# Kernel tuning notes

Hardware: AMD Instinct MI355X
Metric: run time of the kernel (lower is better)

The kernel has to match this reference:

```python
import jax, jax.numpy as jnp
import numpy as np
import math

S, B, F, D, H, L, DFF, PRED = 448, 64, 8, 256, 8, 4, 256, 96
DK = D // H
EPS = 1e-5


def _pos_enc(length, d_model):
    pos = jnp.arange(length, dtype=jnp.float32)[:, None]            # [S,1]
    div = jnp.exp(jnp.arange(0, d_model, 2, dtype=jnp.float32) * (-math.log(10000.0) / d_model))
    pe = jnp.zeros((length, d_model), jnp.float32)
    pe = pe.at[:, 0::2].set(jnp.sin(pos * div))
    pe = pe.at[:, 1::2].set(jnp.cos(pos * div))
    return pe[:, None, :]                                            # [S,1,D]


def _layernorm(x, g, b):
    mu = jnp.mean(x, axis=-1, keepdims=True)
    var = jnp.mean((x - mu) ** 2, axis=-1, keepdims=True)
    return (x - mu) / jnp.sqrt(var + EPS) * g + b


def setup_inputs() -> dict:
    key = jax.random.key(0)
    ks = jax.random.split(key, 12)
    g = lambda k, shape: (jax.random.normal(k, shape) * 0.02).astype(jnp.float32)
    return {
        "src": jax.random.normal(ks[0], (S, B, F), jnp.float32),
        "w_in": g(ks[1], (F, D)), "b_in": jnp.zeros((D,), jnp.float32),
        "Wq": g(ks[2], (L, D, D)), "bq": jnp.zeros((L, D), jnp.float32),
        "Wk": g(ks[3], (L, D, D)), "bk": jnp.zeros((L, D), jnp.float32),
        "Wv": g(ks[4], (L, D, D)), "bv": jnp.zeros((L, D), jnp.float32),
        "Wo": g(ks[5], (L, D, D)), "bo": jnp.zeros((L, D), jnp.float32),
        "g1": jnp.ones((L, D), jnp.float32), "be1": jnp.zeros((L, D), jnp.float32),
        "W1": g(ks[6], (L, D, DFF)), "b1": jnp.zeros((L, DFF), jnp.float32),
        "W2": g(ks[7], (L, DFF, D)), "b2": jnp.zeros((L, D), jnp.float32),
        "g2": jnp.ones((L, D), jnp.float32), "be2": jnp.zeros((L, D), jnp.float32),
        "w_out": g(ks[8], (D, F)), "b_out": jnp.zeros((F,), jnp.float32),
    }


def reference(src, w_in, b_in, Wq, bq, Wk, bk, Wv, bv, Wo, bo,
              g1, be1, W1, b1, W2, b2, g2, be2, w_out, b_out):
    x = src @ w_in + b_in                 # [S,B,D]
    x = x + _pos_enc(S, D)

    scale = math.sqrt(DK)

    def layer(x, p):
        wq, bq_, wk, bk_, wv, bv_, wo, bo_, g1_, be1_, w1, b1_, w2, b2_, g2_, be2_ = p
        Q = (x @ wq + bq_).reshape(S, B, H, DK)
        K = (x @ wk + bk_).reshape(S, B, H, DK)
        V = (x @ wv + bv_).reshape(S, B, H, DK)
        scores = jnp.einsum("sbhd,tbhd->bhst", Q, K) / scale   # [B,H,S,S]
        attn = jax.nn.softmax(scores, axis=-1)
        ctx = jnp.einsum("bhst,tbhd->sbhd", attn, V).reshape(S, B, D)
        x = _layernorm(x + (ctx @ wo + bo_), g1_, be1_)
        ff = jax.nn.relu(x @ w1 + b1_) @ w2 + b2_
        x = _layernorm(x + ff, g2_, be2_)
        return x, None

    x, _ = jax.lax.scan(layer, x, (Wq, bq, Wk, bk, Wv, bv, Wo, bo,
                                   g1, be1, W1, b1, W2, b2, g2, be2))
    return x[-PRED:] @ w_out + b_out      # [PRED,B,F]
```

## Files before the change

### kernel.cpp

```cpp
#include <hip/hip_runtime.h>
#include <hip/hip_bf16.h>
#include <math.h>

#define S_ 448
#define B_ 64
#define F_ 8
#define D_ 256
#define H_ 8
#define DK_ 32
#define L_ 4
#define PRED_ 96
#define NT_ (S_ * B_)
#define PANEL_ (S_ * DK_)
#define VTP_ (32 * 512)
#define SCQ_ 0.25503484f

typedef unsigned short bf16_t;
using bf16x8 = __attribute__((ext_vector_type(8))) short;
using f32x4  = __attribute__((ext_vector_type(4))) float;
using f32x16 = __attribute__((ext_vector_type(16))) float;

__device__ __forceinline__ float b2f(bf16_t b) {
  return __uint_as_float(((unsigned)b) << 16);
}
__device__ __forceinline__ bf16_t f2b(float f) {
  unsigned u = __float_as_uint(f);
  u += 0x7fffu + ((u >> 16) & 1u);
  return (bf16_t)(u >> 16);
}
__device__ __forceinline__ unsigned pk2(float lo, float hi) {
  union { __hip_bfloat162 h; unsigned u; } c;
  c.h = __float22bfloat162_rn(make_float2(lo, hi));
  return c.u;
}
__device__ __forceinline__ void gload16(const bf16_t* g, char* l) {
  __builtin_amdgcn_global_load_lds(
      (const __attribute__((address_space(1))) unsigned*)g,
      (__attribute__((address_space(3))) unsigned*)l, 16, 0, 0);
}

__global__ __launch_bounds__(256) void embed_kernel(
    const float* __restrict__ src, const float* __restrict__ w_in,
    const float* __restrict__ b_in, bf16_t* __restrict__ x) {
  int n = blockIdx.x;
  int d = threadIdx.x;
  const float* srow = src + (size_t)n * F_;
  float acc = b_in[d];
#pragma unroll
  for (int f = 0; f < F_; ++f) acc += srow[f] * w_in[f * D_ + d];
  int s = n / B_;
  int i2 = d & ~1;
  float freq = __expf(-9.210340371976184f * (float)i2 / (float)D_);
  float ang = (float)s * freq;
  float pe = (d & 1) ? cosf(ang) : sinf(ang);
  x[(size_t)n * D_ + d] = f2b(acc + pe);
}

__global__ __launch_bounds__(256) void transpose_w_kernel(
    const float* __restrict__ W, bf16_t* __restrict__ Wt, float scale) {
  __shared__ float t[32][33];
  int l = blockIdx.z;
  int k0 = blockIdx.x * 32, n0 = blockIdx.y * 32;
  int x = threadIdx.x, y = threadIdx.y;
  const float* src = W + ((size_t)l * 256 + k0) * 256 + n0;
#pragma unroll
  for (int i = y; i < 32; i += 8) t[i][x] = src[(size_t)i * 256 + x];
  __syncthreads();
  bf16_t* dst = Wt + ((size_t)l * 256 + n0) * 256 + k0;
#pragma unroll
  for (int i = y; i < 32; i += 8) dst[(size_t)i * 256 + x] = f2b(t[x][i] * scale);
}

__global__ __launch_bounds__(512) void vtrans_kernel(
    const bf16_t* __restrict__ V, bf16_t* __restrict__ Vt) {
  __shared__ bf16_t t[32][456];
  int bh = blockIdx.x, tid = threadIdx.x;
  const bf16_t* Vp = V + (size_t)bh * PANEL_;
#pragma unroll
  for (int p = 0; p < 4; ++p) {
    int idx = tid + p * 512;
    if (idx < 1792) {
      int s = idx >> 2, c = idx & 3;
      uint4 v = *(const uint4*)(Vp + s * 32 + c * 8);
      unsigned w[4] = {v.x, v.y, v.z, v.w};
#pragma unroll
      for (int e = 0; e < 8; ++e) {
        bf16_t val = (bf16_t)((e & 1) ? (w[e >> 1] >> 16) : (w[e >> 1] & 0xffff));
        *(bf16_t*)((char*)&t[0][0] + (c * 8 + e) * 912 + s * 2) = val;
      }
    }
  }
  __syncthreads();
  bf16_t* Op = Vt + (size_t)bh * VTP_;
#pragma unroll
  for (int p = 0; p < 4; ++p) {
    int idx = tid + p * 512;
    int dk = idx >> 6, sl = idx & 63;
    uint4 v = {0, 0, 0, 0};
    if (sl < 56) v = *(const uint4*)((char*)&t[0][0] + dk * 912 + sl * 16);
    *(uint4*)(Op + dk * 512 + sl * 8) = v;
  }
}

template <int ALAY, int OLAY, int RELU>
__device__ __forceinline__ void gemm_body(
    const bf16_t* __restrict__ A, const bf16_t* __restrict__ Wt,
    const float* __restrict__ bias, float bscale, bf16_t* __restrict__ Y,
    int m0, int n0) {
  __shared__ bf16_t As[2][128][32];
  __shared__ bf16_t Bs[2][128][32];
  int tid = threadIdx.x, lane = tid & 63, wv = tid >> 6;
  int wr = wv >> 2, wc = wv & 3;
  int jg = lane >> 4, fr = lane & 15;
  int s_row = tid >> 2;
  int s_p = tid & 3;

  auto stage = [&](int kt, int buf) {
    int k0 = kt * 32;
    int ls = s_p ^ ((s_row >> 1) & 3);
    const bf16_t* ap;
    if (ALAY == 0) {
      ap = A + (size_t)(m0 + s_row) * 256 + k0 + ls * 8;
    } else {
      int n = m0 + s_row;
      int k = k0 + ls * 8;
      ap = A + ((size_t)(((n & 63) << 3) | (k >> 5)) * S_ + (n >> 6)) * DK_ +
           (k & 31);
    }
    const bf16_t* bp = Wt + (size_t)(n0 + s_row) * 256 + k0 + ls * 8;
    gload16(ap, (char*)As + buf * 8192 + wv * 1024);
    gload16(bp, (char*)Bs + buf * 8192 + wv * 1024);
  };

  f32x4 zero = {0.f, 0.f, 0.f, 0.f};
  f32x4 acc[4][2];
#pragma unroll
  for (int i = 0; i < 4; ++i)
#pragma unroll
    for (int j = 0; j < 2; ++j) acc[i][j] = zero;

  stage(0, 0);
  __syncthreads();

  for (int kt = 0; kt < 8; ++kt) {
    int buf = kt & 1;
    if (kt < 7) stage(kt + 1, buf ^ 1);
    bf16x8 af[4], bfr[2];
#pragma unroll
    for (int mi = 0; mi < 4; ++mi) {
      int row = wr * 64 + mi * 16 + fr;
      af[mi] = *(const bf16x8*)((const char*)&As[buf][0][0] + row * 64 +
                                ((jg ^ ((row >> 1) & 3)) << 4));
    }
#pragma unroll
    for (int ni = 0; ni < 2; ++ni) {
      int rn = wc * 32 + ni * 16 + fr;
      bfr[ni] = *(const bf16x8*)((const char*)&Bs[buf][0][0] + rn * 64 +
                                 ((jg ^ ((rn >> 1) & 3)) << 4));
    }
#pragma unroll
    for (int mi = 0; mi < 4; ++mi)
#pragma unroll
      for (int ni = 0; ni < 2; ++ni)
        acc[mi][ni] = __builtin_amdgcn_mfma_f32_16x16x32_bf16(
            af[mi], bfr[ni], acc[mi][ni], 0, 0, 0);
    __syncthreads();
  }

  char* ep0 = (char*)&As[0][0][0] + wv * 1024;
  float bcol[2];
#pragma unroll
  for (int ni = 0; ni < 2; ++ni)
    bcol[ni] = bias[n0 + wc * 32 + ni * 16 + fr] * bscale;
#pragma unroll
  for (int mi = 0; mi < 4; ++mi) {
    char* ep = ep0 + (mi & 1) * 8192;
#pragma unroll
    for (int ni = 0; ni < 2; ++ni)
#pragma unroll
      for (int r = 0; r < 4; ++r) {
        float v = acc[mi][ni][r] + bcol[ni];
        if (RELU) v = fmaxf(v, 0.f);
        int row = jg * 4 + r;
        int cb = (ni * 16 + fr) * 2;
        *(bf16_t*)(ep + row * 64 + (cb ^ (jg << 4))) = f2b(v);
      }
    int row16 = lane >> 2, c = lane & 3;
    uint4 v = *(uint4*)(ep + row16 * 64 +
                        ((c << 4) ^ (((row16 >> 2) & 3) << 4)));
    int n = m0 + wr * 64 + mi * 16 + row16;
    if (OLAY == 0) {
      *(uint4*)((char*)(Y + (size_t)n * 256 + n0 + wc * 32) + c * 16) = v;
    } else {
      int h = (n0 + wc * 32) >> 5;
      *(uint4*)((char*)(Y + ((size_t)(((n & 63) << 3) | h) * S_ + (n >> 6)) *
                                DK_) +
                c * 16) = v;
    }
  }
}

__global__ __launch_bounds__(512, 4) void gemm_qkv_kernel(
    const bf16_t* __restrict__ A, const bf16_t* __restrict__ wq,
    const bf16_t* __restrict__ wk, const bf16_t* __restrict__ wvp,
    const float* __restrict__ bq, const float* __restrict__ bk,
    const float* __restrict__ bvp, bf16_t* __restrict__ yq,
    bf16_t* __restrict__ yk, bf16_t* __restrict__ yv) {
  int bid = blockIdx.x;
  int w = (bid & 7) * 168 + (bid >> 3);
  int sel = w % 6;
  int m0 = (w / 6) * 128;
  int mtx = sel >> 1;
  const bf16_t* W = mtx == 0 ? wq : mtx == 1 ? wk : wvp;
  const float* bb = mtx == 0 ? bq : mtx == 1 ? bk : bvp;
  bf16_t* Y = mtx == 0 ? yq : mtx == 1 ? yk : yv;
  float bscale = mtx == 0 ? SCQ_ : 1.0f;
  gemm_body<0, 1, 0>(A, W, bb, bscale, Y, m0, (sel & 1) * 128);
}

__global__ __launch_bounds__(512, 4) void gemm_relu_kernel(
    const bf16_t* __restrict__ A, const bf16_t* __restrict__ Wt,
    const float* __restrict__ bias, bf16_t* __restrict__ Y) {
  int bid = blockIdx.x;
  int w = (bid & 7) * 56 + (bid >> 3);
  gemm_body<0, 0, 1>(A, Wt, bias, 1.0f, Y, (w >> 1) * 128, (w & 1) * 128);
}

template <int ALAY>
__global__ __launch_bounds__(512, 2) void gemm_ln_kernel(
    const bf16_t* __restrict__ A, const bf16_t* __restrict__ Wt,
    const float* __restrict__ bias, const float* __restrict__ g,
    const float* __restrict__ be, bf16_t* __restrict__ x) {
  __shared__ char smem[40960];
  int tid = threadIdx.x, lane = tid & 63, wv = tid >> 6;
  int wr = wv >> 2, wc = wv & 3;
  int jg = lane >> 4, fr = lane & 15;
  int bid = blockIdx.x;
  int m0 = ((bid & 7) * 56 + (bid >> 3)) * 64;

  auto stage = [&](int kt, int buf) {
    int k0 = kt * 32;
    if (tid < 256) {
      int row = tid >> 2, p = tid & 3;
      int ls = p ^ ((row >> 1) & 3);
      const bf16_t* ap;
      if (ALAY == 0) {
        ap = A + (size_t)(m0 + row) * 256 + k0 + ls * 8;
      } else {
        int n = m0 + row;
        int k = k0 + ls * 8;
        ap = A + ((size_t)(((n & 63) << 3) | (k >> 5)) * S_ + (n >> 6)) * DK_ +
             (k & 31);
      }
      gload16(ap, smem + buf * 4096 + wv * 1024);
    }
    int p = tid & 3;
    int r0 = tid >> 2, r1 = 128 + (tid >> 2);
    gload16(Wt + (size_t)r0 * 256 + k0 + (p ^ ((r0 >> 1) & 3)) * 8,
            smem + 8192 + buf * 16384 + wv * 1024);
    gload16(Wt + (size_t)r1 * 256 + k0 + (p ^ ((r1 >> 1) & 3)) * 8,
            smem + 8192 + buf * 16384 + 8192 + wv * 1024);
  };

  f32x4 zero = {0.f, 0.f, 0.f, 0.f};
  f32x4 acc[2][4];
#pragma unroll
  for (int i = 0; i < 2; ++i)
#pragma unroll
    for (int j = 0; j < 4; ++j) acc[i][j] = zero;

  stage(0, 0);
  __syncthreads();

  for (int kt = 0; kt < 8; ++kt) {
    int buf = kt & 1;
    if (kt < 7) stage(kt + 1, buf ^ 1);
    bf16x8 af[2], bfr[4];
#pragma unroll
    for (int mi = 0; mi < 2; ++mi) {
      int row = wr * 32 + mi * 16 + fr;
      af[mi] = *(const bf16x8*)(smem + buf * 4096 + row * 64 +
                                ((jg ^ ((row >> 1) & 3)) << 4));
    }
#pragma unroll
    for (int ni = 0; ni < 4; ++ni) {
      int rn = wc * 64 + ni * 16 + fr;
      bfr[ni] = *(const bf16x8*)(smem + 8192 + buf * 16384 + rn * 64 +
                                 ((jg ^ ((rn >> 1) & 3)) << 4));
    }
#pragma unroll
    for (int mi = 0; mi < 2; ++mi)
#pragma unroll
      for (int ni = 0; ni < 4; ++ni)
        acc[mi][ni] = __builtin_amdgcn_mfma_f32_16x16x32_bf16(
            af[mi], bfr[ni], acc[mi][ni], 0, 0, 0);
    __syncthreads();
  }

  float* ssum = (float*)smem;
  float* ssq  = (float*)(smem + 1024);
  float* rowm = (float*)(smem + 2048);
  float* rowr = (float*)(smem + 2304);

  float bcol[4], gv[4], bev[4];
#pragma unroll
  for (int ni = 0; ni < 4; ++ni) {
    int c = wc * 64 + ni * 16 + fr;
    bcol[ni] = bias[c];
    gv[ni] = g[c];
    bev[ni] = be[c];
  }
#pragma unroll
  for (int mi = 0; mi < 2; ++mi)
#pragma unroll
    for (int r = 0; r < 4; ++r) {
      int row = wr * 32 + mi * 16 + jg * 4 + r;
      size_t gbase = (size_t)(m0 + row) * 256 + wc * 64 + fr;
      float s = 0.f, s2 = 0.f;
#pragma unroll
      for (int ni = 0; ni < 4; ++ni) {
        float v = acc[mi][ni][r] + bcol[ni] + b2f(x[gbase + ni * 16]);
        acc[mi][ni][r] = v;
        s += v;
        s2 += v * v;
      }
#pragma unroll
      for (int off = 1; off <= 8; off <<= 1) {
        s += __shfl_xor(s, off);
        s2 += __shfl_xor(s2, off);
      }
      if (fr == 0) {
        ssum[row * 4 + wc] = s;
        ssq[row * 4 + wc] = s2;
      }
    }
  __syncthreads();
  if (tid < 64) {
    float s = ssum[tid * 4] + ssum[tid * 4 + 1] + ssum[tid * 4 + 2] +
              ssum[tid * 4 + 3];
    float q = ssq[tid * 4] + ssq[tid * 4 + 1] + ssq[tid * 4 + 2] +
              ssq[tid * 4 + 3];
    float mean = s * (1.f / 256.f);
    float var = q * (1.f / 256.f) - mean * mean;
    rowm[tid] = mean;
    rowr[tid] = rsqrtf(var + 1e-5f);
  }
  __syncthreads();
  char* ep0 = smem + 8192 + wv * 2048;
#pragma unroll
  for (int mi = 0; mi < 2; ++mi) {
    char* ep = ep0 + mi * 16384;
#pragma unroll
    for (int r = 0; r < 4; ++r) {
      int row = wr * 32 + mi * 16 + jg * 4 + r;
      float mean = rowm[row], rinv = rowr[row];
#pragma unroll
      for (int ni = 0; ni < 4; ++ni) {
        float lnv = (acc[mi][ni][r] - mean) * rinv * gv[ni] + bev[ni];
        int cb = (ni * 16 + fr) * 2;
        *(bf16_t*)(ep + (jg * 4 + r) * 128 + (cb ^ (jg << 4))) = f2b(lnv);
      }
    }
    int row16 = lane >> 2;
#pragma unroll
    for (int ps = 0; ps < 2; ++ps) {
      int ch = (lane & 3) + ps * 4;
      uint4 v = *(uint4*)(ep + row16 * 128 + ((ch * 16) ^ ((row16 >> 2) << 4)));
      *(uint4*)(x + (size_t)(m0 + wr * 32 + mi * 16 + row16) * 256 + wc * 64 +
                ch * 8) = v;
    }
  }
}

__global__ __launch_bounds__(448) void attn_v6_kernel(
    bf16_t* __restrict__ Q, const bf16_t* __restrict__ K,
    const bf16_t* __restrict__ Vt) {
  __shared__ char Ep[7][2560];
  int tid = threadIdx.x, lane = tid & 63, wv = tid >> 6;
  int bh = blockIdx.x;
  bf16_t* Qp = Q + (size_t)bh * PANEL_;
  const bf16_t* Kp = K + (size_t)bh * PANEL_;
  const bf16_t* Vp = Vt + (size_t)bh * VTP_;
  int lo31 = lane & 31, hi = lane >> 5;
  const f32x16 z16 = {0.f, 0.f, 0.f, 0.f, 0.f, 0.f, 0.f, 0.f,
                      0.f, 0.f, 0.f, 0.f, 0.f, 0.f, 0.f, 0.f};
  int q0a = wv * 32, q0b = q0a + 224;

  bf16x8 qa0 = *(const bf16x8*)(Qp + (q0a + lo31) * 32 + hi * 8);
  bf16x8 qa1 = *(const bf16x8*)(Qp + (q0a + lo31) * 32 + 16 + hi * 8);
  bf16x8 qb0 = *(const bf16x8*)(Qp + (q0b + lo31) * 32 + hi * 8);
  bf16x8 qb1 = *(const bf16x8*)(Qp + (q0b + lo31) * 32 + 16 + hi * 8);

  float mA = -3.0e38f, lA = 0.f, mB = -3.0e38f, lB = 0.f;
  f32x16 oA = z16, oB = z16;

#define PV_SUB(SV, RB, TOFF, OD)                                              \
  {                                                                           \
    unsigned a0 = pk2(SV[RB + 0], SV[RB + 1]);                                \
    unsigned a1 = pk2(SV[RB + 2], SV[RB + 3]);                                \
    unsigned b0 = pk2(SV[RB + 4], SV[RB + 5]);                                \
    unsigned b1 = pk2(SV[RB + 6], SV[RB + 7]);                                \
    unsigned xa0 = (unsigned)__shfl_xor((int)a0, 32);                         \
    unsigned xa1 = (unsigned)__shfl_xor((int)a1, 32);                         \
    unsigned xb0 = (unsigned)__shfl_xor((int)b0, 32);                         \
    unsigned xb1 = (unsigned)__shfl_xor((int)b1, 32);                         \
    union { unsigned u[4]; bf16x8 v; } pf;                                    \
    pf.u[0] = hi ? xb0 : a0;                                                  \
    pf.u[1] = hi ? xb1 : a1;                                                  \
    pf.u[2] = hi ? b0 : xa0;                                                  \
    pf.u[3] = hi ? b1 : xa1;                                                  \
    bf16x8 vf = *(const bf16x8*)(Vp + lo31 * 512 + (TOFF) + hi * 8);          \
    OD = __builtin_amdgcn_mfma_f32_32x32x16_bf16(pf.v, vf, OD, 0, 0, 0);      \
  }

  for (int kc = 0; kc < 14; ++kc) {
    int t0 = kc * 32;
    const bf16_t* kr = Kp + (t0 + lo31) * 32 + hi * 8;
    bf16x8 k0 = *(const bf16x8*)(kr);
    bf16x8 k1 = *(const bf16x8*)(kr + 16);
    f32x16 sA = z16, sB = z16;
    __builtin_amdgcn_s_setprio(1);
    sA = __builtin_amdgcn_mfma_f32_32x32x16_bf16(k0, qa0, sA, 0, 0, 0);
    sA = __builtin_amdgcn_mfma_f32_32x32x16_bf16(k1, qa1, sA, 0, 0, 0);
    sB = __builtin_amdgcn_mfma_f32_32x32x16_bf16(k0, qb0, sB, 0, 0, 0);
    sB = __builtin_amdgcn_mfma_f32_32x32x16_bf16(k1, qb1, sB, 0, 0, 0);
    __builtin_amdgcn_s_setprio(0);

    {
      float cm = -3.0e38f;
#pragma unroll
      for (int r = 0; r < 16; ++r) cm = fmaxf(cm, sA[r]);
      cm = fmaxf(cm, __shfl_xor(cm, 32));
      if (!__all(cm <= mA + 8.0f)) {
        float mn = fmaxf(mA, cm);
        float sc = exp2f(mA - mn);
        lA *= sc;
#pragma unroll
        for (int r = 0; r < 16; ++r) oA[r] *= sc;
        mA = mn;
      }
      float ls = 0.f;
#pragma unroll
      for (int r = 0; r < 16; ++r) {
        float p = exp2f(sA[r] - mA);
        sA[r] = p;
        ls += p;
      }
      ls += __shfl_xor(ls, 32);
      lA += ls;
    }
    {
      float cm = -3.0e38f;
#pragma unroll
      for (int r = 0; r < 16; ++r) cm = fmaxf(cm, sB[r]);
      cm = fmaxf(cm, __shfl_xor(cm, 32));
      if (!__all(cm <= mB + 8.0f)) {
        float mn = fmaxf(mB, cm);
        float sc = exp2f(mB - mn);
        lB *= sc;
#pragma unroll
        for (int r = 0; r < 16; ++r) oB[r] *= sc;
        mB = mn;
      }
      float ls = 0.f;
#pragma unroll
      for (int r = 0; r < 16; ++r) {
        float p = exp2f(sB[r] - mB);
        sB[r] = p;
        ls += p;
      }
      ls += __shfl_xor(ls, 32);
      lB += ls;
    }
    PV_SUB(sA, 0, t0, oA)
    PV_SUB(sA, 8, t0 + 16, oA)
    PV_SUB(sB, 0, t0, oB)
    PV_SUB(sB, 8, t0 + 16, oB)
  }
#undef PV_SUB

  char* ep = &Ep[wv][0];
#pragma unroll
  for (int tt = 0; tt < 2; ++tt) {
    float l_run = tt ? lB : lA;
    int q0 = tt ? q0b : q0a;
    float inv = 1.f / l_run;
#pragma unroll
    for (int r = 0; r < 16; ++r) {
      int q = (r & 3) + 8 * (r >> 2) + 4 * hi;
      float iq = __shfl(inv, q);
      float ov = tt ? oB[r] : oA[r];
      *(bf16_t*)(ep + q * 80 + lo31 * 2) = f2b(ov * iq);
    }
#pragma unroll
    for (int ps = 0; ps < 2; ++ps) {
      int row = ps * 16 + (lane >> 2), ch = lane & 3;
      uint4 v = *(uint4*)(ep + row * 80 + ch * 16);
      *(uint4*)(Qp + (q0 + row) * 32 + ch * 8) = v;
    }
  }
}

__global__ __launch_bounds__(512) void attn_v3f_kernel(
    bf16_t* __restrict__ Q, const bf16_t* __restrict__ K,
    const bf16_t* __restrict__ Vsrc) {
  __shared__ bf16_t Vt[32][520];
  __shared__ char Pbuf[8][2048];
  int tid = threadIdx.x, lane = tid & 63, wv = tid >> 6;
  int bid = blockIdx.x;
  int bh = (bid & 7) | ((bid >> 5) << 3);
  int chunk = (bid >> 3) & 3;
  bf16_t* Qp = Q + (size_t)bh * PANEL_;
  const bf16_t* Kp = K + (size_t)bh * PANEL_;
  int jg = lane >> 4, fr = lane & 15;

  const bf16_t* Vp = Vsrc + (size_t)bh * PANEL_;
  for (int idx = tid; idx < 448 * 4; idx += 512) {
    int t = idx >> 2, c = idx & 3;
    uint4 vv = *(const uint4*)(Vp + t * 32 + c * 8);
    unsigned w[4] = {vv.x, vv.y, vv.z, vv.w};
#pragma unroll
    for (int e = 0; e < 8; ++e) {
      bf16_t val = (bf16_t)((e & 1) ? (w[e >> 1] >> 16) : (w[e >> 1] & 0xffff));
      *(bf16_t*)((char*)&Vt[0][0] + (c * 8 + e) * 1040 + t * 2) = val;
    }
  }
  __syncthreads();

  int q0 = chunk * 128 + wv * 16;
  if (q0 < S_) {
    f32x4 zero = {0.f, 0.f, 0.f, 0.f};
    bf16x8 qf = *(const bf16x8*)(Qp + (q0 + fr) * 32 + jg * 8);
    f32x4 s2[28];
#pragma unroll
    for (int ct = 0; ct < 28; ++ct) {
      bf16x8 kf = *(const bf16x8*)(Kp + (ct * 16 + fr) * 32 + jg * 8);
      s2[ct] = __builtin_amdgcn_mfma_f32_16x16x32_bf16(kf, qf, zero, 0, 0, 0);
    }
    float m = s2[0][0];
#pragma unroll
    for (int ct = 0; ct < 28; ++ct)
#pragma unroll
      for (int r = 0; r < 4; ++r) m = fmaxf(m, s2[ct][r]);
    m = fmaxf(m, __shfl_xor(m, 16));
    m = fmaxf(m, __shfl_xor(m, 32));
    float l = 0.f;
#pragma unroll
    for (int ct = 0; ct < 28; ++ct)
#pragma unroll
      for (int r = 0; r < 4; ++r) {
        float p = exp2f(s2[ct][r] - m);
        s2[ct][r] = p;
        l += p;
      }
    l += __shfl_xor(l, 16);
    l += __shfl_xor(l, 32);
    float inv = 1.f / l;

    char* pb0 = &Pbuf[wv][0];
    f32x4 o[2] = {zero, zero};
#pragma unroll
    for (int c = 0; c < 14; ++c) {
      char* pb = pb0 + (c & 1) * 1024;
      uint2 w0, w1;
      w0.x = pk2(s2[2 * c][0], s2[2 * c][1]);
      w0.y = pk2(s2[2 * c][2], s2[2 * c][3]);
      w1.x = pk2(s2[2 * c + 1][0], s2[2 * c + 1][1]);
      w1.y = pk2(s2[2 * c + 1][2], s2[2 * c + 1][3]);
      *(uint2*)(pb + fr * 64 + 8 * jg) = w0;
      *(uint2*)(pb + fr * 64 + 32 + 8 * jg) = w1;
      bf16x8 pf = *(const bf16x8*)(pb + fr * 64 + jg * 16);
#pragma unroll
      for (int nt = 0; nt < 2; ++nt) {
        bf16x8 vf = *(const bf16x8*)((const char*)&Vt[0][0] +
                                     (nt * 16 + fr) * 1040 +
                                     (c * 32 + jg * 8) * 2);
        o[nt] = __builtin_amdgcn_mfma_f32_16x16x32_bf16(pf, vf, o[nt], 0, 0, 0);
      }
    }
    float invq[4];
#pragma unroll
    for (int r = 0; r < 4; ++r) invq[r] = __shfl(inv, jg * 4 + r);
#pragma unroll
    for (int nt = 0; nt < 2; ++nt)
#pragma unroll
      for (int r = 0; r < 4; ++r) {
        float v = o[nt][r] * invq[r];
        int row = jg * 4 + r;
        int cb = (nt * 16 + fr) * 2;
        *(bf16_t*)(pb0 + row * 64 + (cb ^ (jg << 4))) = f2b(v);
      }
    {
      int row16 = lane >> 2, c = lane & 3;
      uint4 v = *(uint4*)(pb0 + row16 * 64 +
                          ((c << 4) ^ (((row16 >> 2) & 3) << 4)));
      *(uint4*)(Qp + (q0 + row16) * 32 + c * 8) = v;
    }
  }
}

__global__ __launch_bounds__(256) void out_kernel(
    const bf16_t* __restrict__ x, const float* __restrict__ w_out,
    const float* __restrict__ b_out, float* __restrict__ out) {
  int idx = blockIdx.x * 256 + threadIdx.x;
  int f = idx & 7;
  int pb = idx >> 3;
  const bf16_t* xrow = x + ((size_t)(S_ - PRED_) * B_ + pb) * D_;
  float acc = b_out[f];
  for (int dd = 0; dd < D_; ++dd) acc += b2f(xrow[dd]) * w_out[dd * F_ + f];
  out[idx] = acc;
}

extern "C" void kernel_launch(void* const* d_in, const int* in_sizes, int n_in,
                              void* d_out, int out_size, void* d_ws, size_t ws_size,
                              hipStream_t stream) {
  const float* src  = (const float*)d_in[0];
  const float* w_in = (const float*)d_in[1];
  const float* b_in = (const float*)d_in[2];
  const float* Wq = (const float*)d_in[3];
  const float* bq = (const float*)d_in[4];
  const float* Wk = (const float*)d_in[5];
  const float* bk = (const float*)d_in[6];
  const float* Wv = (const float*)d_in[7];
  const float* bv = (const float*)d_in[8];
  const float* Wo = (const float*)d_in[9];
  const float* bo = (const float*)d_in[10];
  const float* g1 = (const float*)d_in[11];
  const float* be1 = (const float*)d_in[12];
  const float* W1 = (const float*)d_in[13];
  const float* b1 = (const float*)d_in[14];
  const float* W2 = (const float*)d_in[15];
  const float* b2 = (const float*)d_in[16];
  const float* g2 = (const float*)d_in[17];
  const float* be2 = (const float*)d_in[18];
  const float* w_out = (const float*)d_in[19];
  const float* b_out = (const float*)d_in[20];
  float* out = (float*)d_out;

  const size_t NTD = (size_t)NT_ * D_;
  bf16_t* xb = (bf16_t*)d_ws;
  bf16_t* qb = xb + NTD;
  bf16_t* kb = qb + NTD;
  bf16_t* vb = kb + NTD;
  bf16_t* wt = vb + NTD;
  const size_t WSZ = (size_t)L_ * 65536;
  bf16_t* wtq = wt;
  bf16_t* wtk = wtq + WSZ;
  bf16_t* wtv = wtk + WSZ;
  bf16_t* wto = wtv + WSZ;
  bf16_t* wt1 = wto + WSZ;
  bf16_t* wt2 = wt1 + WSZ;
  bf16_t* vtb = wt2 + WSZ;

  const size_t NEED = ((size_t)4 * NTD + 6 * WSZ + (size_t)512 * VTP_) * 2;
  const int use_vt = (ws_size >= NEED) ? 1 : 0;

  dim3 tb(32, 8), tg(8, 8, L_);
  transpose_w_kernel<<<tg, tb, 0, stream>>>(Wq, wtq, SCQ_);
  transpose_w_kernel<<<tg, tb, 0, stream>>>(Wk, wtk, 1.0f);
  transpose_w_kernel<<<tg, tb, 0, stream>>>(Wv, wtv, 1.0f);
  transpose_w_kernel<<<tg, tb, 0, stream>>>(Wo, wto, 1.0f);
  transpose_w_kernel<<<tg, tb, 0, stream>>>(W1, wt1, 1.0f);
  transpose_w_kernel<<<tg, tb, 0, stream>>>(W2, wt2, 1.0f);

  embed_kernel<<<NT_, 256, 0, stream>>>(src, w_in, b_in, xb);

  for (int l = 0; l < L_; ++l) {
    const size_t woff = (size_t)l * 65536;
    const size_t boff = (size_t)l * D_;
    gemm_qkv_kernel<<<1344, 512, 0, stream>>>(
        xb, wtq + woff, wtk + woff, wtv + woff, bq + boff, bk + boff,
        bv + boff, qb, kb, vb);
    if (use_vt) {
      vtrans_kernel<<<512, 512, 0, stream>>>(vb, vtb);
      attn_v6_kernel<<<512, 448, 0, stream>>>(qb, kb, vtb);
    } else {
      attn_v3f_kernel<<<2048, 512, 0, stream>>>(qb, kb, vb);
    }
    gemm_ln_kernel<1><<<448, 512, 0, stream>>>(qb, wto + woff, bo + boff,
                                               g1 + boff, be1 + boff, xb);
    gemm_relu_kernel<<<448, 512, 0, stream>>>(xb, wt1 + woff, b1 + boff, qb);
    gemm_ln_kernel<0><<<448, 512, 0, stream>>>(qb, wt2 + woff, b2 + boff,
                                               g2 + boff, be2 + boff, xb);
  }

  out_kernel<<<(PRED_ * B_ * F_) / 256, 256, 0, stream>>>(xb, w_out, b_out, out);
}
```

Baseline: 525.8 us.

## Split attention query tiles across two blocks per head with K/V register prefetch

New measurement: 527.6 us. About the same (+0.3%).

```diff
diff --git a/kernel.cpp b/kernel.cpp
--- a/kernel.cpp
+++ b/kernel.cpp
@@ -372,132 +372,125 @@
   }
 }
 
-__global__ __launch_bounds__(448) void attn_v6_kernel(
+__global__ __launch_bounds__(448) void attn_v7_kernel(
     bf16_t* __restrict__ Q, const bf16_t* __restrict__ K,
     const bf16_t* __restrict__ Vt) {
   __shared__ char Ep[7][2560];
   int tid = threadIdx.x, lane = tid & 63, wv = tid >> 6;
-  int bh = blockIdx.x;
+  int bid = blockIdx.x;
+  int xcd = bid & 7, j = bid >> 3;
+  int bh = ((j >> 1) << 3) | xcd;
+  int half = j & 1;
+  int q0 = (half * 7 + wv) * 32;
   bf16_t* Qp = Q + (size_t)bh * PANEL_;
   const bf16_t* Kp = K + (size_t)bh * PANEL_;
   const bf16_t* Vp = Vt + (size_t)bh * VTP_;
   int lo31 = lane & 31, hi = lane >> 5;
   const f32x16 z16 = {0.f, 0.f, 0.f, 0.f, 0.f, 0.f, 0.f, 0.f,
                       0.f, 0.f, 0.f, 0.f, 0.f, 0.f, 0.f, 0.f};
-  int q0a = wv * 32, q0b = q0a + 224;
-
-  bf16x8 qa0 = *(const bf16x8*)(Qp + (q0a + lo31) * 32 + hi * 8);
-  bf16x8 qa1 = *(const bf16x8*)(Qp + (q0a + lo31) * 32 + 16 + hi * 8);
-  bf16x8 qb0 = *(const bf16x8*)(Qp + (q0b + lo31) * 32 + hi * 8);
-  bf16x8 qb1 = *(const bf16x8*)(Qp + (q0b + lo31) * 32 + 16 + hi * 8);
-
-  float mA = -3.0e38f, lA = 0.f, mB = -3.0e38f, lB = 0.f;
-  f32x16 oA = z16, oB = z16;
-
-#define PV_SUB(SV, RB, TOFF, OD)                                              \
+
+  bf16x8 qf0 = *(const bf16x8*)(Qp + (q0 + lo31) * 32 + hi * 8);
+  bf16x8 qf1 = *(const bf16x8*)(Qp + (q0 + lo31) * 32 + 16 + hi * 8);
+
+  const bf16_t* kr = Kp + lo31 * 32 + hi * 8;
+  const bf16_t* vr = Vp + lo31 * 512 + hi * 8;
+
+  float m_run = -3.0e38f, l_run = 0.f;
+  f32x16 o = z16;
+
+#define CHUNK(K0, K1, V0, V1)                                                 \
   {                                                                           \
-    unsigned a0 = pk2(SV[RB + 0], SV[RB + 1]);                                \
-    unsigned a1 = pk2(SV[RB + 2], SV[RB + 3]);                                \
-    unsigned b0 = pk2(SV[RB + 4], SV[RB + 5]);                                \
-    unsigned b1 = pk2(SV[RB + 6], SV[RB + 7]);                                \
-    unsigned xa0 = (unsigned)__shfl_xor((int)a0, 32);                         \
-    unsigned xa1 = (unsigned)__shfl_xor((int)a1, 32);                         \
-    unsigned xb0 = (unsigned)__shfl_xor((int)b0, 32);                         \
-    unsigned xb1 = (unsigned)__shfl_xor((int)b1, 32);                         \
-    union { unsigned u[4]; bf16x8 v; } pf;                                    \
-    pf.u[0] = hi ? xb0 : a0;                                                  \
-    pf.u[1] = hi ? xb1 : a1;                                                  \
-    pf.u[2] = hi ? b0 : xa0;                                                  \
-    pf.u[3] = hi ? b1 : xa1;                                                  \
-    bf16x8 vf = *(const bf16x8*)(Vp + lo31 * 512 + (TOFF) + hi * 8);          \
-    OD = __builtin_amdgcn_mfma_f32_32x32x16_bf16(pf.v, vf, OD, 0, 0, 0);      \
-  }
-
-  for (int kc = 0; kc < 14; ++kc) {
-    int t0 = kc * 32;
-    const bf16_t* kr = Kp + (t0 + lo31) * 32 + hi * 8;
-    bf16x8 k0 = *(const bf16x8*)(kr);
-    bf16x8 k1 = *(const bf16x8*)(kr + 16);
-    f32x16 sA = z16, sB = z16;
-    __builtin_amdgcn_s_setprio(1);
-    sA = __builtin_amdgcn_mfma_f32_32x32x16_bf16(k0, qa0, sA, 0, 0, 0);
-    sA = __builtin_amdgcn_mfma_f32_32x32x16_bf16(k1, qa1, sA, 0, 0, 0);
-    sB = __builtin_amdgcn_mfma_f32_32x32x16_bf16(k0, qb0, sB, 0, 0, 0);
-    sB = __builtin_amdgcn_mfma_f32_32x32x16_bf16(k1, qb1, sB, 0, 0, 0);
-    __builtin_amdgcn_s_setprio(0);
-
-    {
-      float cm = -3.0e38f;
-#pragma unroll
-      for (int r = 0; r < 16; ++r) cm = fmaxf(cm, sA[r]);
-      cm = fmaxf(cm, __shfl_xor(cm, 32));
-      if (!__all(cm <= mA + 8.0f)) {
-        float mn = fmaxf(mA, cm);
-        float sc = exp2f(mA - mn);
-        lA *= sc;
-#pragma unroll
-        for (int r = 0; r < 16; ++r) oA[r] *= sc;
-        mA = mn;
-      }
-      float ls = 0.f;
-#pragma unroll
-      for (int r = 0; r < 16; ++r) {
-        float p = exp2f(sA[r] - mA);
-        sA[r] = p;
-        ls += p;
-      }
-      ls += __shfl_xor(ls, 32);
-      lA += ls;
-    }
-    {
-      float cm = -3.0e38f;
-#pragma unroll
-      for (int r = 0; r < 16; ++r) cm = fmaxf(cm, sB[r]);
-      cm = fmaxf(cm, __shfl_xor(cm, 32));
-      if (!__all(cm <= mB + 8.0f)) {
-        float mn = fmaxf(mB, cm);
-        float sc = exp2f(mB - mn);
-        lB *= sc;
-#pragma unroll
-        for (int r = 0; r < 16; ++r) oB[r] *= sc;
-        mB = mn;
-      }
-      float ls = 0.f;
-#pragma unroll
-      for (int r = 0; r < 16; ++r) {
-        float p = exp2f(sB[r] - mB);
-        sB[r] = p;
-        ls += p;
-      }
-      ls += __shfl_xor(ls, 32);
-      lB += ls;
-    }
-    PV_SUB(sA, 0, t0, oA)
-    PV_SUB(sA, 8, t0 + 16, oA)
-    PV_SUB(sB, 0, t0, oB)
-    PV_SUB(sB, 8, t0 + 16, oB)
-  }
-#undef PV_SUB
-
+    f32x16 s = z16;                                                           \
+    __builtin_amdgcn_s_setprio(1);                                            \
+    s = __builtin_amdgcn_mfma_f32_32x32x16_bf16(K0, qf0, s, 0, 0, 0);         \
+    s = __builtin_amdgcn_mfma_f32_32x32x16_bf16(K1, qf1, s, 0, 0, 0);         \
+    __builtin_amdgcn_s_setprio(0);                                            \
+    float cm = -3.0e38f;                                                      \
+    _Pragma("unroll") for (int r = 0; r < 16; ++r) cm = fmaxf(cm, s[r]);      \
+    cm = fmaxf(cm, __shfl_xor(cm, 32));                                       \
+    if (!__all(cm <= m_run + 8.0f)) {                                         \
+      float mn = fmaxf(m_run, cm);                                            \
+      float sc = exp2f(m_run - mn);                                           \
+      l_run *= sc;                                                            \
+      _Pragma("unroll") for (int r = 0; r < 16; ++r) o[r] *= sc;              \
+      m_run = mn;                                                             \
+    }                                                                         \
+    float ls = 0.f;                                                           \
+    _Pragma("unroll") for (int r = 0; r < 16; ++r) {                          \
+      float p = exp2f(s[r] - m_run);                                          \
+      s[r] = p;                                                               \
+      ls += p;                                                                \
+    }                                                                         \
+    ls += __shfl_xor(ls, 32);                                                 \
+    l_run += ls;                                                              \
+    {                                                                         \
+      unsigned a0 = pk2(s[0], s[1]), a1 = pk2(s[2], s[3]);                    \
+      unsigned b0 = pk2(s[4], s[5]), b1 = pk2(s[6], s[7]);                    \
+      unsigned xa0 = (unsigned)__shfl_xor((int)a0, 32);                       \
+      unsigned xa1 = (unsigned)__shfl_xor((int)a1, 32);                       \
+      unsigned xb0 = (unsigned)__shfl_xor((int)b0, 32);                       \
+      unsigned xb1 = (unsigned)__shfl_xor((int)b1, 32);                       \
+      union { unsigned u[4]; bf16x8 v; } pf;                                  \
+      pf.u[0] = hi ? xb0 : a0;                                                \
+      pf.u[1] = hi ? xb1 : a1;                                                \
+      pf.u[2] = hi ? b0 : xa0;                                                \
+      pf.u[3] = hi ? b1 : xa1;                                                \
+      o = __builtin_amdgcn_mfma_f32_32x32x16_bf16(pf.v, V0, o, 0, 0, 0);      \
+    }                                                                         \
+    {                                                                         \
+      unsigned a0 = pk2(s[8], s[9]), a1 = pk2(s[10], s[11]);                  \
+      unsigned b0 = pk2(s[12], s[13]), b1 = pk2(s[14], s[15]);                \
+      unsigned xa0 = (unsigned)__shfl_xor((int)a0, 32);                       \
+      unsigned xa1 = (unsigned)__shfl_xor((int)a1, 32);                       \
+      unsigned xb0 = (unsigned)__shfl_xor((int)b0, 32);                       \
+      unsigned xb1 = (unsigned)__shfl_xor((int)b1, 32);                       \
+      union { unsigned u[4]; bf16x8 v; } pf;                                  \
+      pf.u[0] = hi ? xb0 : a0;                                                \
+      pf.u[1] = hi ? xb1 : a1;                                                \
+      pf.u[2] = hi ? b0 : xa0;                                                \
+      pf.u[3] = hi ? b1 : xa1;                                                \
+      o = __builtin_amdgcn_mfma_f32_32x32x16_bf16(pf.v, V1, o, 0, 0, 0);      \
+    }                                                                         \
+  }
+
+  bf16x8 ck0 = *(const bf16x8*)(kr);
+  bf16x8 ck1 = *(const bf16x8*)(kr + 16);
+  bf16x8 cv0 = *(const bf16x8*)(vr);
+  bf16x8 cv1 = *(const bf16x8*)(vr + 16);
+
+  for (int kc = 0; kc < 14; kc += 2) {
+    const bf16_t* krn = kr + (kc + 1) * 1024;
+    const bf16_t* vrn = vr + (kc + 1) * 32;
+    bf16x8 nk0 = *(const bf16x8*)(krn);
+    bf16x8 nk1 = *(const bf16x8*)(krn + 16);
+    bf16x8 nv0 = *(const bf16x8*)(vrn);
+    bf16x8 nv1 = *(const bf16x8*)(vrn + 16);
+    CHUNK(ck0, ck1, cv0, cv1)
+    if (kc + 2 < 14) {
+      const bf16_t* krm = kr + (kc + 2) * 1024;
+      const bf16_t* vrm = vr + (kc + 2) * 32;
+      ck0 = *(const bf16x8*)(krm);
+      ck1 = *(const bf16x8*)(krm + 16);
+      cv0 = *(const bf16x8*)(vrm);
+      cv1 = *(const bf16x8*)(vrm + 16);
+    }
+    CHUNK(nk0, nk1, nv0, nv1)
+  }
+#undef CHUNK
+
+  float inv = 1.f / l_run;
   char* ep = &Ep[wv][0];
 #pragma unroll
-  for (int tt = 0; tt < 2; ++tt) {
-    float l_run = tt ? lB : lA;
-    int q0 = tt ? q0b : q0a;
-    float inv = 1.f / l_run;
-#pragma unroll
-    for (int r = 0; r < 16; ++r) {
-      int q = (r & 3) + 8 * (r >> 2) + 4 * hi;
-      float iq = __shfl(inv, q);
-      float ov = tt ? oB[r] : oA[r];
-      *(bf16_t*)(ep + q * 80 + lo31 * 2) = f2b(ov * iq);
-    }
-#pragma unroll
-    for (int ps = 0; ps < 2; ++ps) {
-      int row = ps * 16 + (lane >> 2), ch = lane & 3;
-      uint4 v = *(uint4*)(ep + row * 80 + ch * 16);
-      *(uint4*)(Qp + (q0 + row) * 32 + ch * 8) = v;
-    }
+  for (int r = 0; r < 16; ++r) {
+    int q = (r & 3) + 8 * (r >> 2) + 4 * hi;
+    float iq = __shfl(inv, q);
+    *(bf16_t*)(ep + q * 80 + lo31 * 2) = f2b(o[r] * iq);
+  }
+#pragma unroll
+  for (int ps = 0; ps < 2; ++ps) {
+    int row = ps * 16 + (lane >> 2), ch = lane & 3;
+    uint4 v = *(uint4*)(ep + row * 80 + ch * 16);
+    *(uint4*)(Qp + (q0 + row) * 32 + ch * 8) = v;
   }
 }
 
@@ -673,7 +666,7 @@
         bv + boff, qb, kb, vb);
     if (use_vt) {
       vtrans_kernel<<<512, 512, 0, stream>>>(vb, vtb);
-      attn_v6_kernel<<<512, 448, 0, stream>>>(qb, kb, vtb);
+      attn_v7_kernel<<<1024, 448, 0, stream>>>(qb, kb, vtb);
     } else {
       attn_v3f_kernel<<<2048, 512, 0, stream>>>(qb, kb, vb);
     }
```
